# Performance work log

Measured on AMD Instinct MI355X. Metric: run time of the kernel, lower is better.

## Reference

```python
import jax, jax.numpy as jnp
import numpy as np

B, N, M = 16, 1024, 4
D = 128          # embedding_dim == nhid
VOCAB = 32000
HOPS = 3
HEADS = 4
LAYERS = 1
ALPHA = 0.2
NEG_INF = -9e15


def setup_inputs() -> dict:
    key = jax.random.key(0)
    ks = jax.random.split(key, 10)
    story = jax.random.randint(ks[0], (B, N, M), 0, VOCAB)
    kb_len = jax.random.randint(ks[1], (B,), 1, N // 2 + 1)
    conv_len = jax.random.randint(ks[2], (B,), 1, N // 2)
    hidden = jax.random.normal(ks[3], (B, D), dtype=jnp.float32)
    dh_outputs = jax.random.normal(ks[4], (B, N, D), dtype=jnp.float32)
    adj = (jax.random.uniform(ks[5], (B, N, N)) < 0.02).astype(jnp.float32)
    # learned params
    emb = 0.1 * jax.random.normal(ks[6], (HOPS + 1, VOCAB, D), dtype=jnp.float32)
    lim = 1.0 / np.sqrt(D)
    gat_W = jax.random.uniform(ks[7], (LAYERS, HOPS + 1, HEADS, D, D), minval=-lim, maxval=lim, dtype=jnp.float32)
    gat_a = jax.random.uniform(ks[8], (LAYERS, HOPS + 1, HEADS, 2 * D), minval=-lim, maxval=lim, dtype=jnp.float32)
    return {"story": story, "kb_len": kb_len, "conv_len": conv_len,
            "hidden": hidden, "dh_outputs": dh_outputs, "adj": adj,
            "emb": emb, "gat_W": gat_W, "gat_a": gat_a}


def _forward(story, kb_len, conv_len, hidden, dh_outputs, adj, emb, gat_W, gat_a):
    pos = jnp.arange(N)
    # update_pad_token_adj: self-loop for padded slots k >= (kb_len-1)+conv_len+1
    ctx = kb_len + conv_len                                  # [B]
    diag_fix = (pos[None, :] >= ctx[:, None]).astype(adj.dtype)  # [B,N]
    adj = jnp.maximum(adj, jnp.eye(N, dtype=adj.dtype)[None] * diag_fix[:, :, None])
    adj_mask = adj > 0                                       # [B,N,N]

    def add_lm(mem):
        # scatter dh_outputs[b, :conv_len[b]] into rows [kb_len[b]-1, kb_len[b]-1+conv_len[b])
        start = kb_len - 1                                   # [B]
        rel = pos[None, :] - start[:, None]                  # [B,N]
        within = (rel >= 0) & (rel < conv_len[:, None])
        gath = jnp.take_along_axis(dh_outputs, jnp.clip(rel, 0, N - 1)[:, :, None], axis=1)
        return mem + jnp.where(within[:, :, None], gath, 0.0)

    def gat_stack(x, hop_idx):
        out = x
        for l in range(LAYERS):
            W = gat_W[l, hop_idx]                            # [H,D,E]
            a = gat_a[l, hop_idx]                            # [H,2E]
            E = W.shape[-1]
            Wh = jnp.einsum('bnd,hde->hbne', out, W)         # [H,B,N,E]
            f1 = jnp.einsum('hbne,he->hbn', Wh, a[:, :E])
            f2 = jnp.einsum('hbne,he->hbn', Wh, a[:, E:])
            e = jax.nn.leaky_relu(f1[..., None] + f2[..., None, :], ALPHA)  # [H,B,N,N]
            e = jnp.where(adj_mask[None], e, NEG_INF)
            att = jax.nn.softmax(e, axis=-1)
            out = jnp.einsum('hbnm,hbme->bne', att, Wh) / HEADS  # head-mean (concat=False)
        return out

    def embed(hop_idx):
        x = jnp.sum(emb[hop_idx][story], axis=2)             # [B,N,M,D] -> [B,N,D]
        return add_lm(x)

    u = hidden
    prob_logits = None
    for hop in range(HOPS):
        A = gat_stack(embed(hop), hop)
        prob_logits = jnp.einsum('bnd,bd->bn', A, u)
        prob_soft = jax.nn.softmax(prob_logits, axis=1)
        Cm = gat_stack(embed(hop + 1), hop + 1)
        u = u + jnp.einsum('bnd,bn->bd', Cm, prob_soft)
    return jax.nn.sigmoid(prob_logits), u, prob_logits


def reference(story, kb_len, conv_len, hidden, dh_outputs, adj, emb, gat_W, gat_a):
    return _forward(story, kb_len, conv_len, hidden, dh_outputs, adj, emb, gat_W, gat_a)
```

## Files before the change

### kernel.cpp

```cpp
#include <hip/hip_runtime.h>
#include <hip/hip_bf16.h>
#include <math.h>

#define Bz 16
#define Nz 1024
#define Mz 4
#define Dz 128
#define Hz 4
#define VOCABz 32000
#define CAP 128
#define BNc (Bz * Nz)
#define NC 576

typedef __attribute__((ext_vector_type(8))) short bf16x8;
typedef __attribute__((ext_vector_type(4))) float f32x4;
typedef __attribute__((ext_vector_type(2))) _Float16 f16x2;

#if defined(__has_builtin)
#if __has_builtin(__builtin_amdgcn_fdot2)
#define FDOT2(w, s, acc) acc = __builtin_amdgcn_fdot2((w), (s), (acc), false)
#endif
#endif
#ifndef FDOT2
#define FDOT2(w, s, acc) acc += (float)(w)[0] * (float)(s)[0] + (float)(w)[1] * (float)(s)[1]
#endif

__device__ inline unsigned short rne_bf16(float x) {
    unsigned u = __float_as_uint(x);
    unsigned r = (u + 0x7FFFu + ((u >> 16) & 1u)) >> 16;
    return (unsigned short)r;
}
__device__ inline float bf16_to_f(unsigned short h) {
    return __uint_as_float(((unsigned)h) << 16);
}
__device__ inline unsigned short f32_to_f16_bits(float x) {
    _Float16 hv = (_Float16)x;
    return __builtin_bit_cast(unsigned short, hv);
}

__global__ __launch_bounds__(256) void k_prep(const float* __restrict__ adj,
                                              const int* __restrict__ kb_len,
                                              const int* __restrict__ conv_len,
                                              const float* __restrict__ gat_W,
                                              const float* __restrict__ gat_a,
                                              const float* __restrict__ hidden,
                                              int* __restrict__ idx, int* __restrict__ cnt,
                                              unsigned short* __restrict__ wthi,
                                              unsigned short* __restrict__ wtlo,
                                              float* __restrict__ u) {
    int blk = blockIdx.x;
    int t = threadIdx.x;
    if (blk < BNc) {
        int row = blk;
        int b = row >> 10, n = row & 1023;
        __shared__ int scnt;
        if (t == 0) scnt = 0;
        __syncthreads();
        int ctx = kb_len[b] + conv_len[b];
        const float4 av = *((const float4*)(adj + (size_t)row * Nz) + t);
        int m0 = t * 4;
#pragma unroll
        for (int k = 0; k < 4; k++) {
            float a = k == 0 ? av.x : k == 1 ? av.y : k == 2 ? av.z : av.w;
            int m = m0 + k;
            bool on = (a > 0.f) || (m == n && n >= ctx);
            if (on) {
                int p = atomicAdd(&scnt, 1);
                if (p < CAP) idx[(size_t)row * CAP + p] = m;
            }
        }
        __syncthreads();
        if (t == 0) cnt[row] = scnt < CAP ? scnt : CAP;
    } else if (blk < BNc + 1152) {
        int i = (blk - BNc) * 256 + t;
        int d = i & 127;
        int rest = i >> 7;
        int c = rest % NC;
        int hop = rest / NC;
        float v;
        if (c < 512) {
            int h = c & 3, e = c >> 2;
            v = gat_W[(((size_t)(hop * 4 + h)) * 128 + d) * 128 + e];
        } else if (c < 520) {
            int q = c - 512;
            int h = q & 3, which = q >> 2;
            const float* wrow = gat_W + (((size_t)(hop * 4 + h)) * 128 + d) * 128;
            const float* arow = gat_a + ((size_t)(hop * 4 + h)) * 256 + which * 128;
            float s = 0.f;
            for (int e = 0; e < 128; e++) s += wrow[e] * arow[e];
            v = s;
        } else {
            v = 0.f;
        }
        unsigned short h = rne_bf16(v);
        wthi[i] = h;
        wtlo[i] = rne_bf16(v - bf16_to_f(h));
    } else {
        int i = (blk - BNc - 1152) * 256 + t;
        if (i < Bz * Dz) u[i] = hidden[i];
    }
}

__global__ __launch_bounds__(128) void k_embed4(const int* __restrict__ story,
                                                const float* __restrict__ emb,
                                                const float* __restrict__ dh,
                                                const int* __restrict__ kb_len,
                                                const int* __restrict__ conv_len,
                                                unsigned short* __restrict__ xhi,
                                                unsigned short* __restrict__ xlo) {
    int row = blockIdx.x;
    int b = row >> 10, n = row & 1023;
    int d = threadIdx.x;
    const int* st = story + (size_t)row * Mz;
    int s0 = st[0], s1 = st[1], s2 = st[2], s3 = st[3];
    int rel = n - (kb_len[b] - 1);
    float dhv = (rel >= 0 && rel < conv_len[b]) ? dh[((size_t)(b << 10) + rel) * Dz + d] : 0.f;
#pragma unroll
    for (int hop = 0; hop < 4; hop++) {
        const float* ek = emb + (size_t)hop * VOCABz * Dz;
        float acc = ek[(size_t)s0 * Dz + d] + ek[(size_t)s1 * Dz + d]
                  + ek[(size_t)s2 * Dz + d] + ek[(size_t)s3 * Dz + d] + dhv;
        unsigned short hb = rne_bf16(acc);
        size_t o = (size_t)hop * BNc * Dz + (size_t)row * Dz + d;
        xhi[o] = hb;
        xlo[o] = rne_bf16(acc - bf16_to_f(hb));
    }
}

#define AST 72
__global__ __launch_bounds__(256) void k_whf4(const unsigned short* __restrict__ xhi_a,
                                              const unsigned short* __restrict__ xlo_a,
                                              const unsigned short* __restrict__ wthi_a,
                                              const unsigned short* __restrict__ wtlo_a,
                                              unsigned short* __restrict__ WhT_a,
                                              float* __restrict__ ff) {
    int blk = blockIdx.x;
    int xcd = blk & 7;
    int s = blk >> 3;
    int hop = s / 144;
    int r = s - hop * 144;
    int rt = r / 9;
    int ct = r - rt * 9;
    int row0 = (xcd * 16 + rt) * 128;
    int t = threadIdx.x;
    int wave = t >> 6, lane = t & 63;
    int quad = lane >> 4, l16 = lane & 15;

    const unsigned short* xhi = xhi_a + (size_t)hop * BNc * Dz;
    const unsigned short* xlo = xlo_a + (size_t)hop * BNc * Dz;
    const unsigned short* wthi = wthi_a + (size_t)hop * NC * 128;
    const unsigned short* wtlo = wtlo_a + (size_t)hop * NC * 128;

    __shared__ unsigned short Ah[128 * AST], Al[128 * AST];
    __shared__ unsigned short Bh[64 * AST], Bl[64 * AST];

    f32x4 acc[2][4];
#pragma unroll
    for (int mt = 0; mt < 2; mt++)
#pragma unroll
        for (int nt = 0; nt < 4; nt++) acc[mt][nt] = (f32x4)0.f;

    for (int ph = 0; ph < 2; ph++) {
        int kb = ph * 64;
        for (int i = t; i < 1024; i += 256) {
            int rr = i >> 3, c = (i & 7) * 8;
            *(uint4*)&Ah[rr * AST + c] = *(const uint4*)&xhi[(size_t)(row0 + rr) * Dz + kb + c];
            *(uint4*)&Al[rr * AST + c] = *(const uint4*)&xlo[(size_t)(row0 + rr) * Dz + kb + c];
        }
        for (int i = t; i < 512; i += 256) {
            int cr = i >> 3, cc = (i & 7) * 8;
            size_t src = ((size_t)(ct * 64 + cr)) * 128 + kb + cc;
            *(uint4*)&Bh[cr * AST + cc] = *(const uint4*)&wthi[src];
            *(uint4*)&Bl[cr * AST + cc] = *(const uint4*)&wtlo[src];
        }
        __syncthreads();
#pragma unroll
        for (int ks = 0; ks < 2; ks++) {
            int ko = ks * 32 + quad * 8;
            bf16x8 ah[2], al[2];
#pragma unroll
            for (int mt = 0; mt < 2; mt++) {
                int rr = wave * 32 + mt * 16 + l16;
                ah[mt] = *(const bf16x8*)&Ah[rr * AST + ko];
                al[mt] = *(const bf16x8*)&Al[rr * AST + ko];
            }
#pragma unroll
            for (int nt = 0; nt < 4; nt++) {
                int cc = nt * 16 + l16;
                bf16x8 bh = *(const bf16x8*)&Bh[cc * AST + ko];
                bf16x8 bl = *(const bf16x8*)&Bl[cc * AST + ko];
#pragma unroll
                for (int mt = 0; mt < 2; mt++) {
                    acc[mt][nt] = __builtin_amdgcn_mfma_f32_16x16x32_bf16(ah[mt], bh, acc[mt][nt], 0, 0, 0);
                    acc[mt][nt] = __builtin_amdgcn_mfma_f32_16x16x32_bf16(ah[mt], bl, acc[mt][nt], 0, 0, 0);
                    acc[mt][nt] = __builtin_amdgcn_mfma_f32_16x16x32_bf16(al[mt], bh, acc[mt][nt], 0, 0, 0);
                }
            }
        }
        __syncthreads();
    }

    if (ct < 8) {
        unsigned short* St = Ah;
#pragma unroll
        for (int mt = 0; mt < 2; mt++)
#pragma unroll
            for (int nt = 0; nt < 4; nt++)
#pragma unroll
                for (int reg = 0; reg < 4; reg++) {
                    int rr = wave * 32 + mt * 16 + quad * 4 + reg;
                    int cc = nt * 16 + l16;
                    St[rr * AST + cc] = f32_to_f16_bits(acc[mt][nt][reg]);
                }
        __syncthreads();
        int rr = t >> 1, seg = t & 1;
        size_t gbase = ((size_t)hop * BNc + row0 + rr) * 512 + ct * 64 + seg * 32;
#pragma unroll
        for (int k = 0; k < 4; k++) {
            uint4 vv = *(uint4*)&St[rr * AST + seg * 32 + k * 8];
            *(uint4*)&WhT_a[gbase + k * 8] = vv;
        }
    } else {
        if (l16 < 8) {
#pragma unroll
            for (int mt = 0; mt < 2; mt++)
#pragma unroll
                for (int reg = 0; reg < 4; reg++) {
                    int row = row0 + wave * 32 + mt * 16 + quad * 4 + reg;
                    ff[((size_t)hop * BNc + row) * 8 + l16] = acc[mt][0][reg];
                }
        }
    }
}

__global__ __launch_bounds__(128) void k_attn4(const unsigned short* __restrict__ WhT_a,
                                               const float* __restrict__ ff,
                                               const int* __restrict__ idx,
                                               const int* __restrict__ cnt,
                                               float* __restrict__ G_a) {
    int blk = blockIdx.x;
    int xcd = blk & 7;
    int s = blk >> 3;
    int g = s >> 10;
    int n = s & 1023;
    int p = (g << 3) | xcd;
    int hop = p >> 4;
    int b = p & 15;
    int row = (b << 10) | n;
    int t = threadIdx.x;
    __shared__ int sidx[CAP];
    __shared__ float sat[Hz][CAP];
    __shared__ f16x2 sp01[CAP], sp23[CAP];
    __shared__ float red[8];
    int deg = cnt[row];
    const unsigned short* WhTb = WhT_a + ((size_t)hop * BNc + ((size_t)b << 10)) * 512;
    const float* ffh = ff + (size_t)hop * BNc * 8;
    if (deg > 0) {
        if (t < deg) {
            int m = idx[(size_t)row * CAP + t];
            sidx[t] = m;
            int mrow = (b << 10) | m;
            float4 f1r = *(const float4*)&ffh[(size_t)row * 8];
            float4 f2m = *(const float4*)&ffh[(size_t)mrow * 8 + 4];
            float e0v = f1r.x + f2m.x;
            float e1v = f1r.y + f2m.y;
            float e2v = f1r.z + f2m.z;
            float e3v = f1r.w + f2m.w;
            sat[0][t] = e0v >= 0.f ? e0v : 0.2f * e0v;
            sat[1][t] = e1v >= 0.f ? e1v : 0.2f * e1v;
            sat[2][t] = e2v >= 0.f ? e2v : 0.2f * e2v;
            sat[3][t] = e3v >= 0.f ? e3v : 0.2f * e3v;
        }
        __syncthreads();
        int h = t >> 5, j0 = t & 31;
        float mx = -1e30f;
        for (int j = j0; j < deg; j += 32) mx = fmaxf(mx, sat[h][j]);
#pragma unroll
        for (int mm = 1; mm < 32; mm <<= 1) mx = fmaxf(mx, __shfl_xor(mx, mm));
        if (j0 == 0) red[h] = mx;
        __syncthreads();
        mx = red[h];
        float sum = 0.f;
        for (int j = j0; j < deg; j += 32) {
            float v = expf(sat[h][j] - mx);
            sat[h][j] = v;
            sum += v;
        }
#pragma unroll
        for (int mm = 1; mm < 32; mm <<= 1) sum += __shfl_xor(sum, mm);
        if (j0 == 0) red[4 + h] = 0.25f / sum;
        __syncthreads();
        if (t < deg) {
            float s0 = sat[0][t] * red[4];
            float s1 = sat[1][t] * red[5];
            float s2 = sat[2][t] * red[6];
            float s3 = sat[3][t] * red[7];
            f16x2 p01, p23;
            p01[0] = (_Float16)s0; p01[1] = (_Float16)s1;
            p23[0] = (_Float16)s2; p23[1] = (_Float16)s3;
            sp01[t] = p01;
            sp23[t] = p23;
        }
        __syncthreads();
        float acc = 0.f;
        const unsigned short* wb = WhTb + t * 4;
#pragma unroll 4
        for (int j = 0; j < deg; j++) {
            int m = sidx[j];
            uint2 raw = *(const uint2*)(wb + (size_t)m * 512);
            f16x2 w01 = __builtin_bit_cast(f16x2, raw.x);
            f16x2 w23 = __builtin_bit_cast(f16x2, raw.y);
            FDOT2(w01, sp01[j], acc);
            FDOT2(w23, sp23[j], acc);
        }
        G_a[((size_t)hop * BNc + row) * Dz + t] = acc;
    } else {
        float acc = 0.f;
        const unsigned short* wb = WhTb + t * 4;
        for (int m = 0; m < Nz; m++) {
            uint2 raw = *(const uint2*)(wb + (size_t)m * 512);
            f16x2 w01 = __builtin_bit_cast(f16x2, raw.x);
            f16x2 w23 = __builtin_bit_cast(f16x2, raw.y);
            acc += (float)w01[0] + (float)w01[1] + (float)w23[0] + (float)w23[1];
        }
        G_a[((size_t)hop * BNc + row) * Dz + t] = acc * (1.f / (Hz * Nz));
    }
}

__global__ __launch_bounds__(256) void k_logits4(const float* __restrict__ G_a, int hopA,
                                                 const float* __restrict__ u,
                                                 float* __restrict__ logits) {
    int row = blockIdx.x * 4 + (threadIdx.x >> 6);
    int lane = threadIdx.x & 63;
    int b = row >> 10;
    const float* g = G_a + ((size_t)hopA * BNc + row) * Dz;
    const float* ub = u + b * Dz;
    float s = g[lane] * ub[lane] + g[lane + 64] * ub[lane + 64];
#pragma unroll
    for (int off = 32; off; off >>= 1) s += __shfl_down(s, off);
    if (lane == 0) logits[row] = s;
}

__global__ __launch_bounds__(256) void k_upd(const float* __restrict__ G_a, int hopC,
                                             const float* __restrict__ logits,
                                             float* __restrict__ u) {
    int b = blockIdx.x >> 3;
    int chunk = blockIdx.x & 7;
    int t = threadIdx.x;
    __shared__ float sp[1024];
    __shared__ float red[10];
    __shared__ float part[2][128];
    const float* l = logits + (size_t)b * Nz;
    float4 lv = *((const float4*)l + t);
    float mx = fmaxf(fmaxf(lv.x, lv.y), fmaxf(lv.z, lv.w));
#pragma unroll
    for (int mm = 1; mm < 64; mm <<= 1) mx = fmaxf(mx, __shfl_xor(mx, mm));
    if ((t & 63) == 0) red[t >> 6] = mx;
    __syncthreads();
    if (t == 0) {
        float m = red[0];
        for (int i = 1; i < 4; i++) m = fmaxf(m, red[i]);
        red[8] = m;
    }
    __syncthreads();
    mx = red[8];
    float e0 = expf(lv.x - mx), e1 = expf(lv.y - mx), e2 = expf(lv.z - mx), e3 = expf(lv.w - mx);
    float sum = e0 + e1 + e2 + e3;
#pragma unroll
    for (int mm = 1; mm < 64; mm <<= 1) sum += __shfl_xor(sum, mm);
    if ((t & 63) == 0) red[4 + (t >> 6)] = sum;
    __syncthreads();
    if (t == 0) {
        float ss = 0.f;
        for (int i = 0; i < 4; i++) ss += red[4 + i];
        red[9] = 1.f / ss;
    }
    __syncthreads();
    float inv = red[9];
    sp[t * 4] = e0 * inv;
    sp[t * 4 + 1] = e1 * inv;
    sp[t * 4 + 2] = e2 * inv;
    sp[t * 4 + 3] = e3 * inv;
    __syncthreads();
    int d = t & 127, half = t >> 7;
    const float* gc = G_a + ((size_t)hopC * BNc + (b << 10) + chunk * 128 + half * 64) * Dz + d;
    const float* pc = &sp[chunk * 128 + half * 64];
    float acc = 0.f;
#pragma unroll 4
    for (int j = 0; j < 64; j++) acc += gc[(size_t)j * Dz] * pc[j];
    part[half][d] = acc;
    __syncthreads();
    if (t < 128) atomicAdd(&u[b * Dz + t], part[0][t] + part[1][t]);
}

__global__ void k_fin(const float* __restrict__ logits, const float* __restrict__ u,
                      float* __restrict__ out) {
    int i = blockIdx.x * 256 + threadIdx.x;
    if (i < Bz * Nz) {
        float l = logits[i];
        out[i] = 1.f / (1.f + expf(-l));
        out[Bz * Nz + Bz * Dz + i] = l;
    }
    if (i < Bz * Dz) out[Bz * Nz + i] = u[i];
}

extern "C" void kernel_launch(void* const* d_in, const int* in_sizes, int n_in,
                              void* d_out, int out_size, void* d_ws, size_t ws_size,
                              hipStream_t stream) {
    const int*   story    = (const int*)d_in[0];
    const int*   kb_len   = (const int*)d_in[1];
    const int*   conv_len = (const int*)d_in[2];
    const float* hidden   = (const float*)d_in[3];
    const float* dh       = (const float*)d_in[4];
    const float* adj      = (const float*)d_in[5];
    const float* emb      = (const float*)d_in[6];
    const float* gat_W    = (const float*)d_in[7];
    const float* gat_a    = (const float*)d_in[8];
    float* out = (float*)d_out;

    char* w = (char*)d_ws;
    auto alloc = [&](size_t bytes) {
        char* pp = w;
        w += (bytes + 255) & ~(size_t)255;
        return pp;
    };
    const size_t BN = (size_t)Bz * Nz;
    int*            idx  = (int*)           alloc(BN * CAP * 4);
    int*            cnt  = (int*)           alloc(BN * 4);
    unsigned short* xhi  = (unsigned short*)alloc(4 * BN * Dz * 2);
    unsigned short* xlo  = (unsigned short*)alloc(4 * BN * Dz * 2);
    unsigned short* wthi = (unsigned short*)alloc(4 * NC * 128 * 2);
    unsigned short* wtlo = (unsigned short*)alloc(4 * NC * 128 * 2);
    unsigned short* WhT  = (unsigned short*)alloc(4 * BN * 512 * 2);
    float*          ff   = (float*)         alloc(4 * BN * 8 * 4);
    float*          G    = (float*)         alloc(4 * BN * Dz * 4);
    float*          logits = (float*)       alloc(BN * 4);
    float*          u    = (float*)         alloc((size_t)Bz * Dz * 4);

    k_prep<<<BNc + 1152 + 8, 256, 0, stream>>>(adj, kb_len, conv_len, gat_W, gat_a, hidden,
                                               idx, cnt, wthi, wtlo, u);
    k_embed4<<<BNc, 128, 0, stream>>>(story, emb, dh, kb_len, conv_len, xhi, xlo);
    k_whf4<<<4608, 256, 0, stream>>>(xhi, xlo, wthi, wtlo, WhT, ff);
    k_attn4<<<4 * BNc, 128, 0, stream>>>(WhT, ff, idx, cnt, G);
    for (int hop = 0; hop < 3; hop++) {
        k_logits4<<<BNc / 4, 256, 0, stream>>>(G, hop, u, logits);
        k_upd<<<Bz * 8, 256, 0, stream>>>(G, hop + 1, logits, u);
    }
    k_fin<<<(Bz * Nz + 255) / 256, 256, 0, stream>>>(logits, u, out);
}
```

Measured before the change: 367.0 us.

## Process one attention row per wavefront with register softmax and readlane broadcasts

Restructures the sparse GAT attention kernel so each 64-lane wavefront handles one node row and a 256-thread block covers four rows, instead of one 128-thread block per row. The softmax over up to 128 neighbours is done in registers with cross-lane shuffles, and neighbour indices and f16 weights are broadcast with readlane, removing shared memory and block-wide barriers. Each lane now loads 16 bytes (two output columns) per neighbour and writes a float2. The cost is more serial work per wave, a second loop for neighbours beyond 64, and more register pressure.

```diff
diff --git a/kernel.cpp b/kernel.cpp
--- a/kernel.cpp
+++ b/kernel.cpp
@@ -36,6 +36,12 @@
 __device__ inline unsigned short f32_to_f16_bits(float x) {
     _Float16 hv = (_Float16)x;
     return __builtin_bit_cast(unsigned short, hv);
+}
+__device__ inline unsigned pack_f16(float a, float b) {
+    f16x2 p;
+    p[0] = (_Float16)a;
+    p[1] = (_Float16)b;
+    return __builtin_bit_cast(unsigned, p);
 }
 
 __global__ __launch_bounds__(256) void k_prep(const float* __restrict__ adj,
@@ -233,7 +239,7 @@
     }
 }
 
-__global__ __launch_bounds__(128) void k_attn4(const unsigned short* __restrict__ WhT_a,
+__global__ __launch_bounds__(256) void k_attn4(const unsigned short* __restrict__ WhT_a,
                                                const float* __restrict__ ff,
                                                const int* __restrict__ idx,
                                                const int* __restrict__ cnt,
@@ -241,90 +247,103 @@
     int blk = blockIdx.x;
     int xcd = blk & 7;
     int s = blk >> 3;
-    int g = s >> 10;
-    int n = s & 1023;
+    int g = s >> 8;
     int p = (g << 3) | xcd;
-    int hop = p >> 4;
-    int b = p & 15;
+    int hop = p >> 4, b = p & 15;
+    int wid = threadIdx.x >> 6, lane = threadIdx.x & 63;
+    int n = ((s & 255) << 2) | wid;
     int row = (b << 10) | n;
-    int t = threadIdx.x;
-    __shared__ int sidx[CAP];
-    __shared__ float sat[Hz][CAP];
-    __shared__ f16x2 sp01[CAP], sp23[CAP];
-    __shared__ float red[8];
     int deg = cnt[row];
     const unsigned short* WhTb = WhT_a + ((size_t)hop * BNc + ((size_t)b << 10)) * 512;
+    const char* wblc = (const char*)WhTb + lane * 16;
     const float* ffh = ff + (size_t)hop * BNc * 8;
+    float accx = 0.f, accy = 0.f;
     if (deg > 0) {
-        if (t < deg) {
-            int m = idx[(size_t)row * CAP + t];
-            sidx[t] = m;
-            int mrow = (b << 10) | m;
-            float4 f1r = *(const float4*)&ffh[(size_t)row * 8];
-            float4 f2m = *(const float4*)&ffh[(size_t)mrow * 8 + 4];
-            float e0v = f1r.x + f2m.x;
-            float e1v = f1r.y + f2m.y;
-            float e2v = f1r.z + f2m.z;
-            float e3v = f1r.w + f2m.w;
-            sat[0][t] = e0v >= 0.f ? e0v : 0.2f * e0v;
-            sat[1][t] = e1v >= 0.f ? e1v : 0.2f * e1v;
-            sat[2][t] = e2v >= 0.f ? e2v : 0.2f * e2v;
-            sat[3][t] = e3v >= 0.f ? e3v : 0.2f * e3v;
-        }
-        __syncthreads();
-        int h = t >> 5, j0 = t & 31;
-        float mx = -1e30f;
-        for (int j = j0; j < deg; j += 32) mx = fmaxf(mx, sat[h][j]);
-#pragma unroll
-        for (int mm = 1; mm < 32; mm <<= 1) mx = fmaxf(mx, __shfl_xor(mx, mm));
-        if (j0 == 0) red[h] = mx;
-        __syncthreads();
-        mx = red[h];
-        float sum = 0.f;
-        for (int j = j0; j < deg; j += 32) {
-            float v = expf(sat[h][j] - mx);
-            sat[h][j] = v;
-            sum += v;
-        }
-#pragma unroll
-        for (int mm = 1; mm < 32; mm <<= 1) sum += __shfl_xor(sum, mm);
-        if (j0 == 0) red[4 + h] = 0.25f / sum;
-        __syncthreads();
-        if (t < deg) {
-            float s0 = sat[0][t] * red[4];
-            float s1 = sat[1][t] * red[5];
-            float s2 = sat[2][t] * red[6];
-            float s3 = sat[3][t] * red[7];
-            f16x2 p01, p23;
-            p01[0] = (_Float16)s0; p01[1] = (_Float16)s1;
-            p23[0] = (_Float16)s2; p23[1] = (_Float16)s3;
-            sp01[t] = p01;
-            sp23[t] = p23;
-        }
-        __syncthreads();
-        float acc = 0.f;
-        const unsigned short* wb = WhTb + t * 4;
-#pragma unroll 4
-        for (int j = 0; j < deg; j++) {
-            int m = sidx[j];
-            uint2 raw = *(const uint2*)(wb + (size_t)m * 512);
-            f16x2 w01 = __builtin_bit_cast(f16x2, raw.x);
-            f16x2 w23 = __builtin_bit_cast(f16x2, raw.y);
-            FDOT2(w01, sp01[j], acc);
-            FDOT2(w23, sp23[j], acc);
-        }
-        G_a[((size_t)hop * BNc + row) * Dz + t] = acc;
+        int m0 = lane < deg ? idx[(size_t)row * CAP + lane] : -1;
+        int m1 = lane + 64 < deg ? idx[(size_t)row * CAP + lane + 64] : -1;
+        float4 f1r = *(const float4*)&ffh[(size_t)row * 8];
+        int m0c = m0 < 0 ? 0 : m0, m1c = m1 < 0 ? 0 : m1;
+        float4 f2a = *(const float4*)&ffh[((size_t)(b << 10) + m0c) * 8 + 4];
+        float4 f2b = *(const float4*)&ffh[((size_t)(b << 10) + m1c) * 8 + 4];
+        float e0[4], e1[4];
+        e0[0] = f1r.x + f2a.x; e0[1] = f1r.y + f2a.y; e0[2] = f1r.z + f2a.z; e0[3] = f1r.w + f2a.w;
+        e1[0] = f1r.x + f2b.x; e1[1] = f1r.y + f2b.y; e1[2] = f1r.z + f2b.z; e1[3] = f1r.w + f2b.w;
+#pragma unroll
+        for (int h = 0; h < 4; h++) {
+            e0[h] = e0[h] >= 0.f ? e0[h] : 0.2f * e0[h];
+            e1[h] = e1[h] >= 0.f ? e1[h] : 0.2f * e1[h];
+            if (m0 < 0) e0[h] = -1e30f;
+            if (m1 < 0) e1[h] = -1e30f;
+        }
+        float mx[4], sum[4];
+#pragma unroll
+        for (int h = 0; h < 4; h++) {
+            float m = fmaxf(e0[h], e1[h]);
+#pragma unroll
+            for (int mm = 1; mm < 64; mm <<= 1) m = fmaxf(m, __shfl_xor(m, mm));
+            mx[h] = m;
+        }
+        float w0[4], w1[4];
+#pragma unroll
+        for (int h = 0; h < 4; h++) {
+            w0[h] = expf(e0[h] - mx[h]);
+            w1[h] = expf(e1[h] - mx[h]);
+            float sm = w0[h] + w1[h];
+#pragma unroll
+            for (int mm = 1; mm < 64; mm <<= 1) sm += __shfl_xor(sm, mm);
+            sum[h] = sm;
+        }
+#pragma unroll
+        for (int h = 0; h < 4; h++) {
+            float inv = 0.25f / sum[h];
+            w0[h] *= inv;
+            w1[h] *= inv;
+        }
+        unsigned w01_0 = pack_f16(w0[0], w0[1]), w23_0 = pack_f16(w0[2], w0[3]);
+        unsigned w01_1 = pack_f16(w1[0], w1[1]), w23_1 = pack_f16(w1[2], w1[3]);
+        int moff0 = m0c << 10;
+        int moff1 = m1c << 10;
+        int dlo = deg < 64 ? deg : 64;
+#pragma unroll 2
+        for (int j = 0; j < dlo; j++) {
+            int so = __builtin_amdgcn_readlane(moff0, j);
+            unsigned a01 = (unsigned)__builtin_amdgcn_readlane((int)w01_0, j);
+            unsigned a23 = (unsigned)__builtin_amdgcn_readlane((int)w23_0, j);
+            uint4 raw = *(const uint4*)(wblc + so);
+            f16x2 p01 = __builtin_bit_cast(f16x2, a01);
+            f16x2 p23 = __builtin_bit_cast(f16x2, a23);
+            FDOT2(__builtin_bit_cast(f16x2, raw.x), p01, accx);
+            FDOT2(__builtin_bit_cast(f16x2, raw.y), p23, accx);
+            FDOT2(__builtin_bit_cast(f16x2, raw.z), p01, accy);
+            FDOT2(__builtin_bit_cast(f16x2, raw.w), p23, accy);
+        }
+        if (deg > 64) {
+            for (int j = 0; j < deg - 64; j++) {
+                int so = __builtin_amdgcn_readlane(moff1, j);
+                unsigned a01 = (unsigned)__builtin_amdgcn_readlane((int)w01_1, j);
+                unsigned a23 = (unsigned)__builtin_amdgcn_readlane((int)w23_1, j);
+                uint4 raw = *(const uint4*)(wblc + so);
+                f16x2 p01 = __builtin_bit_cast(f16x2, a01);
+                f16x2 p23 = __builtin_bit_cast(f16x2, a23);
+                FDOT2(__builtin_bit_cast(f16x2, raw.x), p01, accx);
+                FDOT2(__builtin_bit_cast(f16x2, raw.y), p23, accx);
+                FDOT2(__builtin_bit_cast(f16x2, raw.z), p01, accy);
+                FDOT2(__builtin_bit_cast(f16x2, raw.w), p23, accy);
+            }
+        }
     } else {
-        float acc = 0.f;
-        const unsigned short* wb = WhTb + t * 4;
         for (int m = 0; m < Nz; m++) {
-            uint2 raw = *(const uint2*)(wb + (size_t)m * 512);
-            f16x2 w01 = __builtin_bit_cast(f16x2, raw.x);
-            f16x2 w23 = __builtin_bit_cast(f16x2, raw.y);
-            acc += (float)w01[0] + (float)w01[1] + (float)w23[0] + (float)w23[1];
-        }
-        G_a[((size_t)hop * BNc + row) * Dz + t] = acc * (1.f / (Hz * Nz));
-    }
+            uint4 raw = *(const uint4*)(wblc + (m << 10));
+            f16x2 a = __builtin_bit_cast(f16x2, raw.x), c = __builtin_bit_cast(f16x2, raw.y);
+            f16x2 d = __builtin_bit_cast(f16x2, raw.z), e = __builtin_bit_cast(f16x2, raw.w);
+            accx += (float)a[0] + (float)a[1] + (float)c[0] + (float)c[1];
+            accy += (float)d[0] + (float)d[1] + (float)e[0] + (float)e[1];
+        }
+        accx *= 1.f / (Hz * Nz);
+        accy *= 1.f / (Hz * Nz);
+    }
+    float2 o = make_float2(accx, accy);
+    *(float2*)&G_a[((size_t)hop * BNc + row) * Dz + lane * 2] = o;
 }
 
 __global__ __launch_bounds__(256) void k_logits4(const float* __restrict__ G_a, int hopA,
@@ -441,7 +460,7 @@
                                                idx, cnt, wthi, wtlo, u);
     k_embed4<<<BNc, 128, 0, stream>>>(story, emb, dh, kb_len, conv_len, xhi, xlo);
     k_whf4<<<4608, 256, 0, stream>>>(xhi, xlo, wthi, wtlo, WhT, ff);
-    k_attn4<<<4 * BNc, 128, 0, stream>>>(WhT, ff, idx, cnt, G);
+    k_attn4<<<16384, 256, 0, stream>>>(WhT, ff, idx, cnt, G);
     for (int hop = 0; hop < 3; hop++) {
         k_logits4<<<BNc / 4, 256, 0, stream>>>(G, hop, u, logits);
         k_upd<<<Bz * 8, 256, 0, stream>>>(G, hop + 1, logits, u);
```

Result: faster. 354.5 us (-3.4%).
